# Performance work log

Measured on AMD Instinct MI355X. Metric: run time of the kernel, lower is better.

Reference implementation:

```python
import jax, jax.numpy as jnp
import numpy as np

QUERY_DIM = 512
KEY_DIM = 512
NUM_HEADS = 16
HEAD_DIM = QUERY_DIM // NUM_HEADS


def setup_inputs() -> dict:
    key = jax.random.key(0)
    ks = jax.random.split(key, 10)
    B, T, S = 4, 2048, 2048
    s_q = 1.0 / np.sqrt(QUERY_DIM)
    s_k = 1.0 / np.sqrt(KEY_DIM)
    return {
        "x": jax.random.normal(ks[0], (B, T, QUERY_DIM), dtype=jnp.float32),
        "context": jax.random.normal(ks[1], (B, S, KEY_DIM), dtype=jnp.float32),
        "Wq": jax.random.normal(ks[2], (QUERY_DIM, QUERY_DIM), dtype=jnp.float32) * s_q,
        "bq": jnp.zeros((QUERY_DIM,), dtype=jnp.float32),
        "Wk": jax.random.normal(ks[3], (KEY_DIM, QUERY_DIM), dtype=jnp.float32) * s_k,
        "bk": jnp.zeros((QUERY_DIM,), dtype=jnp.float32),
        "Wv": jax.random.normal(ks[4], (KEY_DIM, QUERY_DIM), dtype=jnp.float32) * s_k,
        "bv": jnp.zeros((QUERY_DIM,), dtype=jnp.float32),
        "Wo": jax.random.normal(ks[5], (QUERY_DIM, QUERY_DIM), dtype=jnp.float32) * s_q,
        "bo": jnp.zeros((QUERY_DIM,), dtype=jnp.float32),
    }


def reference(x, context, Wq, bq, Wk, bk, Wv, bv, Wo, bo):
    B, T, C = x.shape
    S = context.shape[1]
    H, D = NUM_HEADS, HEAD_DIM
    scale = D ** -0.5
    # projections -> [B, H, T/S, D]
    q = (x @ Wq + bq).reshape(B, T, H, D).transpose(0, 2, 1, 3)
    k = (context @ Wk + bk).reshape(B, S, H, D).transpose(0, 2, 1, 3)
    v = (context @ Wv + bv).reshape(B, S, H, D).transpose(0, 2, 1, 3)
    # explicit attention matrix [B, H, T, S] (faithful to the unfused original)
    attn = jnp.einsum("bhtd,bhsd->bhts", q, k) * scale
    attn = jax.nn.softmax(attn, axis=-1)  # dropout is identity in eval mode
    out = jnp.einsum("bhts,bhsd->bhtd", attn, v)
    out = out.transpose(0, 2, 1, 3).reshape(B, T, C)
    return out @ Wo + bo
```

## Files before the change

kernel.cpp:

```cpp
#include <hip/hip_runtime.h>
#include <hip/hip_bf16.h>
#include <cmath>

typedef __bf16 bf16;
typedef __bf16 bf16x2 __attribute__((ext_vector_type(2)));
typedef __bf16 bf16x4 __attribute__((ext_vector_type(4)));
typedef __bf16 bf16x8 __attribute__((ext_vector_type(8)));
typedef float floatx4 __attribute__((ext_vector_type(4)));

#define MFMA_BF16(a, b, c) __builtin_amdgcn_mfma_f32_16x16x32_bf16((a), (b), (c), 0, 0, 0)

#if defined(__has_builtin)
#if __has_builtin(__builtin_amdgcn_global_load_lds)
#define HAVE_GLL 1
#endif
#if __has_builtin(__builtin_amdgcn_cvt_pk_bf16_f32)
#define HAVE_PKCVT 1
#endif
#endif

__device__ __forceinline__ void stage16(const bf16* g, bf16* ldsbase, int lane) {
#ifdef HAVE_GLL
    __builtin_amdgcn_global_load_lds((const __attribute__((address_space(1))) unsigned int*)g,
                                     (__attribute__((address_space(3))) unsigned int*)ldsbase,
                                     16, 0, 0);
#else
    *(int4*)(ldsbase + lane * 8) = *(const int4*)g;
#endif
}

__device__ __forceinline__ bf16x4 pack4(float e0, float e1, float e2, float e3) {
#ifdef HAVE_PKCVT
    const bf16x2 lo = __builtin_amdgcn_cvt_pk_bf16_f32(e0, e1);
    const bf16x2 hi = __builtin_amdgcn_cvt_pk_bf16_f32(e2, e3);
    bf16x4 o;
    o[0] = lo[0]; o[1] = lo[1]; o[2] = hi[0]; o[3] = hi[1];
    return o;
#else
    bf16x4 o;
    o[0] = (bf16)e0; o[1] = (bf16)e1; o[2] = (bf16)e2; o[3] = (bf16)e3;
    return o;
#endif
}

__device__ __forceinline__ int detect_bf16(const void* x) {
    const unsigned short* u = (const unsigned short*)x;
    const int lane = threadIdx.x & 63;
    const unsigned short w0 = u[4 * lane], w1 = u[4 * lane + 2];
    const int e0 = (w0 >> 7) & 0xFF, e1 = (w1 >> 7) & 0xFF;
    const unsigned long long b0 = __ballot(e0 >= 96 && e0 <= 158);
    const unsigned long long b1 = __ballot(e1 >= 96 && e1 <= 158);
    return (__popcll(b0) + __popcll(b1)) >= 90;
}

struct PrepArgs {
    const void* x;
    const void* ctx;
    const void* W[4];
    const void* bias[4];
    bf16* xc;
    bf16* ctxc;
    bf16* WT[4];
    bf16* biasc;
};

__global__ __launch_bounds__(256) void prep(PrepArgs a) {
    const int tid = threadIdx.x;
    const int f = detect_bf16(a.x);
    const int bid = blockIdx.x;
    if (bid < 1024) {
        const int w = bid >> 8, tileid = bid & 255;
        const int bx = tileid & 15, by = tileid >> 4;
        const void* __restrict__ in = a.W[w];
        bf16* __restrict__ out = a.WT[w];
        __shared__ bf16 tile[32][33];
        const int tx = tid & 31, ty = tid >> 5;
        const int x = bx * 32 + tx;
        const int y0 = by * 32;
#pragma unroll
        for (int yy = ty; yy < 32; yy += 8) {
            const size_t idx = (size_t)(y0 + yy) * 512 + x;
            const float v = f ? (float)((const bf16*)in)[idx] : ((const float*)in)[idx];
            tile[yy][tx] = (bf16)v;
        }
        __syncthreads();
        const int xo = by * 32 + tx;
        const int y1 = bx * 32;
#pragma unroll
        for (int yy = ty; yy < 32; yy += 8)
            out[(size_t)(y1 + yy) * 512 + xo] = tile[tx][yy];
    } else if (bid < 5120) {
        if (f) return;
        const int seg = (bid >= 3072);
        const void* src = seg ? a.ctx : a.x;
        bf16* dst = seg ? a.ctxc : a.xc;
        const int off = (bid - (seg ? 3072 : 1024)) * 256 + tid;
        const float4 p = ((const float4*)src)[2 * off];
        const float4 q = ((const float4*)src)[2 * off + 1];
        bf16x8 o;
        o[0] = (bf16)p.x; o[1] = (bf16)p.y; o[2] = (bf16)p.z; o[3] = (bf16)p.w;
        o[4] = (bf16)q.x; o[5] = (bf16)q.y; o[6] = (bf16)q.z; o[7] = (bf16)q.w;
        *(bf16x8*)(dst + (size_t)off * 8) = o;
    } else {
        for (int e = tid; e < 2048; e += 256) {
            const int seg = e >> 9, off = e & 511;
            const float v =
                f ? (float)((const bf16*)a.bias[seg])[off] : ((const float*)a.bias[seg])[off];
            a.biasc[seg * 512 + off] = (bf16)v;
        }
    }
}

struct QkvArgs {
    const void* xraw;
    const void* ctxraw;
    const bf16* Aconv[3];
    const bf16* Wt[3];
    const bf16* bias;
    bf16* out[3];
    float scale[3];
};

__global__ __launch_bounds__(256) void gemm_qkv(QkvArgs a) {
    __shared__ __align__(16) bf16 lA[128 * 32];
    __shared__ __align__(16) bf16 lB[128 * 32];
    const int z = blockIdx.z;
    const int f = detect_bf16(a.xraw);
    const bf16* __restrict__ A =
        f ? (const bf16*)(z == 0 ? a.xraw : a.ctxraw) : a.Aconv[z];
    const bf16* __restrict__ Wt = a.Wt[z];
    const int tid = threadIdx.x, wave = tid >> 6, lane = tid & 63;
    const int qd = lane >> 4, j = lane & 15;
    const int m0 = blockIdx.x * 128, n0 = blockIdx.y * 128;
    const int wrow = (wave & 1) * 64, wcol = (wave >> 1) * 64;
    const int srow = wave * 16 + (lane >> 2);
    const int scol = (lane & 3) * 8;
    const bf16* agp = A + (size_t)(m0 + srow) * 512 + scol;
    const bf16* bgp = Wt + (size_t)(n0 + srow) * 512 + scol;
    bf16* lA0 = lA + wave * 512;
    bf16* lB0 = lB + wave * 512;

    floatx4 acc[4][4] = {};

    for (int k0 = 0; k0 < 512; k0 += 32) {
        stage16(agp + k0, lA0, lane);
        stage16(agp + k0 + (size_t)64 * 512, lA0 + 64 * 32, lane);
        stage16(bgp + k0, lB0, lane);
        stage16(bgp + k0 + (size_t)64 * 512, lB0 + 64 * 32, lane);
        __syncthreads();
        bf16x8 af[4], bfr[4];
#pragma unroll
        for (int i = 0; i < 4; ++i) {
            af[i] = *(const bf16x8*)(lA + (wrow + i * 16 + j) * 32 + qd * 8);
            bfr[i] = *(const bf16x8*)(lB + (wcol + i * 16 + j) * 32 + qd * 8);
        }
        if (z < 2) {
#pragma unroll
            for (int nt = 0; nt < 4; ++nt)
#pragma unroll
                for (int rf = 0; rf < 4; ++rf)
                    acc[nt][rf] = MFMA_BF16(bfr[nt], af[rf], acc[nt][rf]);
        } else {
#pragma unroll
            for (int rf = 0; rf < 4; ++rf)
#pragma unroll
                for (int nt = 0; nt < 4; ++nt)
                    acc[rf][nt] = MFMA_BF16(af[rf], bfr[nt], acc[rf][nt]);
        }
        __syncthreads();
    }

    const float scale = a.scale[z];
    const bf16* bias = a.bias + z * 512;
    bf16* __restrict__ C = a.out[z];
    if (z < 2) {
#pragma unroll
        for (int nt = 0; nt < 4; ++nt) {
            const int nb = n0 + wcol + nt * 16 + qd * 4;
            const bf16x4 bv4 = *(const bf16x4*)(bias + nb);
            const int h = nb >> 5, d0 = nb & 31;
#pragma unroll
            for (int rf = 0; rf < 4; ++rf) {
                const int m = m0 + wrow + rf * 16 + j;
                const int bb = m >> 11, t = m & 2047;
                bf16x4 pk;
#pragma unroll
                for (int r = 0; r < 4; ++r)
                    pk[r] = (bf16)((acc[nt][rf][r] + (float)bv4[r]) * scale);
                *(bf16x4*)(&C[(((size_t)bb * 16 + h) * 2048 + t) * 32 + d0]) = pk;
            }
        }
    } else {
#pragma unroll
        for (int nt = 0; nt < 4; ++nt) {
            const int n = n0 + wcol + nt * 16 + j;
            const float bv = (float)bias[n];
            const int h = n >> 5, d = n & 31;
#pragma unroll
            for (int rf = 0; rf < 4; ++rf) {
                const int t0 = m0 + wrow + rf * 16 + qd * 4;
                const int bb = t0 >> 11, s = t0 & 2047;
                bf16x4 pk;
#pragma unroll
                for (int r = 0; r < 4; ++r) pk[r] = (bf16)(acc[rf][nt][r] + bv);
                *(bf16x4*)(&C[(((size_t)bb * 16 + h) * 32 + d) * 2048 + s]) = pk;
            }
        }
    }
}

__global__ __launch_bounds__(256) void attn_kernel(const bf16* __restrict__ Q,
                                                   const bf16* __restrict__ Kh,
                                                   const bf16* __restrict__ Vt,
                                                   bf16* __restrict__ O) {
    const int tid = threadIdx.x;
    const int wave = tid >> 6, lane = tid & 63;
    const int qd = lane >> 4, j = lane & 15;
    const int bh = blockIdx.x;
    const int b = bh >> 4, h = bh & 15;
    const int tw = blockIdx.y * 256 + wave * 64;

    __shared__ __align__(16) bf16 lP[4][2 * 64 * 68];
    bf16* lp0 = lP[wave];
    bf16* lp1 = lP[wave] + 64 * 68;

    const bf16* qbase = Q + ((size_t)bh * 2048 + tw) * 32;
    const bf16* kbase = Kh + (size_t)bh * 2048 * 32;
    const bf16* vbase = Vt + (size_t)bh * 32 * 2048;

    bf16x8 qf[4];
#pragma unroll
    for (int tf = 0; tf < 4; ++tf)
        qf[tf] = *(const bf16x8*)(qbase + (size_t)(tf * 16 + j) * 32 + qd * 8);

    bf16x8 ones;
#pragma unroll
    for (int e = 0; e < 8; ++e) ones[e] = (bf16)1.0f;

    const floatx4 zero = {0.f, 0.f, 0.f, 0.f};
    floatx4 oacc[4][2] = {};
    floatx4 dacc[4] = {};

    bf16x8 K0[4], K1[4], V0[4], V1[4];

    auto loadK = [&](int s0, bf16x8* k) {
#pragma unroll
        for (int sf = 0; sf < 4; ++sf)
            k[sf] = *(const bf16x8*)(kbase + (size_t)(s0 + sf * 16 + j) * 32 + qd * 8);
    };
    auto loadV = [&](int s0, bf16x8* v) {
#pragma unroll
        for (int dt = 0; dt < 2; ++dt)
#pragma unroll
            for (int kk = 0; kk < 2; ++kk)
                v[dt * 2 + kk] =
                    *(const bf16x8*)(vbase + (size_t)(dt * 16 + j) * 2048 + s0 + kk * 32 + qd * 8);
    };
    auto qk = [&](bf16x8* k, bf16* lp) {
#pragma unroll
        for (int sf = 0; sf < 4; ++sf)
#pragma unroll
            for (int tf = 0; tf < 4; ++tf) {
                const floatx4 sc = MFMA_BF16(k[sf], qf[tf], zero);
                const float e0 = __builtin_amdgcn_exp2f(sc[0]);
                const float e1 = __builtin_amdgcn_exp2f(sc[1]);
                const float e2 = __builtin_amdgcn_exp2f(sc[2]);
                const float e3 = __builtin_amdgcn_exp2f(sc[3]);
                *(bf16x4*)(lp + (tf * 16 + j) * 68 + sf * 16 + qd * 4) = pack4(e0, e1, e2, e3);
            }
    };
    auto pv = [&](bf16x8* v, const bf16* lp) {
#pragma unroll
        for (int rf = 0; rf < 4; ++rf)
#pragma unroll
            for (int kk = 0; kk < 2; ++kk) {
                const bf16x8 pf = *(const bf16x8*)(lp + (rf * 16 + j) * 68 + kk * 32 + qd * 8);
#pragma unroll
                for (int dt = 0; dt < 2; ++dt)
                    oacc[rf][dt] = MFMA_BF16(pf, v[dt * 2 + kk], oacc[rf][dt]);
                dacc[rf] = MFMA_BF16(pf, ones, dacc[rf]);
            }
    };

    loadK(0, K0);
    loadV(0, V0);
    qk(K0, lp0);
    loadK(64, K1);
    for (int it = 0; it < 15; ++it) {
        loadV((2 * it + 1) * 64, V1);
        pv(V0, lp0);
        qk(K1, lp1);
        loadK((2 * it + 2) * 64, K0);
        loadV((2 * it + 2) * 64, V0);
        pv(V1, lp1);
        qk(K0, lp0);
        loadK((2 * it + 3) * 64, K1);
    }
    loadV(31 * 64, V1);
    pv(V0, lp0);
    qk(K1, lp1);
    pv(V1, lp1);

#pragma unroll
    for (int rf = 0; rf < 4; ++rf)
#pragma unroll
        for (int r = 0; r < 4; ++r) {
            const float inv = 1.0f / dacc[rf][r];
            const int t = tw + rf * 16 + qd * 4 + r;
#pragma unroll
            for (int dt = 0; dt < 2; ++dt)
                O[((size_t)b * 2048 + t) * 512 + h * 32 + dt * 16 + j] =
                    (bf16)(oacc[rf][dt][r] * inv);
        }
}

__global__ __launch_bounds__(256) void gemm_out(const bf16* __restrict__ A,
                                                const bf16* __restrict__ Wt,
                                                const bf16* __restrict__ bias,
                                                void* __restrict__ C,
                                                const void* __restrict__ xraw) {
    __shared__ __align__(16) bf16 lA[128 * 32];
    __shared__ __align__(16) bf16 lB[128 * 32];
    const int oflag = detect_bf16(xraw);
    const int tid = threadIdx.x, wave = tid >> 6, lane = tid & 63;
    const int qd = lane >> 4, j = lane & 15;
    const int m0 = blockIdx.x * 128, n0 = blockIdx.y * 128;
    const int wrow = (wave & 1) * 64, wcol = (wave >> 1) * 64;
    const int srow = wave * 16 + (lane >> 2);
    const int scol = (lane & 3) * 8;
    const bf16* agp = A + (size_t)(m0 + srow) * 512 + scol;
    const bf16* bgp = Wt + (size_t)(n0 + srow) * 512 + scol;
    bf16* lA0 = lA + wave * 512;
    bf16* lB0 = lB + wave * 512;

    floatx4 acc[4][4] = {};

    for (int k0 = 0; k0 < 512; k0 += 32) {
        stage16(agp + k0, lA0, lane);
        stage16(agp + k0 + (size_t)64 * 512, lA0 + 64 * 32, lane);
        stage16(bgp + k0, lB0, lane);
        stage16(bgp + k0 + (size_t)64 * 512, lB0 + 64 * 32, lane);
        __syncthreads();
        bf16x8 af[4], bfr[4];
#pragma unroll
        for (int i = 0; i < 4; ++i) {
            af[i] = *(const bf16x8*)(lA + (wrow + i * 16 + j) * 32 + qd * 8);
            bfr[i] = *(const bf16x8*)(lB + (wcol + i * 16 + j) * 32 + qd * 8);
        }
#pragma unroll
        for (int nt = 0; nt < 4; ++nt)
#pragma unroll
            for (int rf = 0; rf < 4; ++rf)
                acc[nt][rf] = MFMA_BF16(bfr[nt], af[rf], acc[nt][rf]);
        __syncthreads();
    }

#pragma unroll
    for (int nt = 0; nt < 4; ++nt) {
        const int nb = n0 + wcol + nt * 16 + qd * 4;
        const bf16x4 bv4 = *(const bf16x4*)(bias + nb);
#pragma unroll
        for (int rf = 0; rf < 4; ++rf) {
            const int m = m0 + wrow + rf * 16 + j;
            if (oflag) {
                bf16x4 pk;
#pragma unroll
                for (int r = 0; r < 4; ++r) pk[r] = (bf16)(acc[nt][rf][r] + (float)bv4[r]);
                *(bf16x4*)((bf16*)C + (size_t)m * 512 + nb) = pk;
            } else {
                float4 v;
                v.x = acc[nt][rf][0] + (float)bv4[0];
                v.y = acc[nt][rf][1] + (float)bv4[1];
                v.z = acc[nt][rf][2] + (float)bv4[2];
                v.w = acc[nt][rf][3] + (float)bv4[3];
                *(float4*)((float*)C + (size_t)m * 512 + nb) = v;
            }
        }
    }
}

extern "C" void kernel_launch(void* const* d_in, const int* in_sizes, int n_in, void* d_out,
                              int out_size, void* d_ws, size_t ws_size, hipStream_t stream) {
    char* ws = (char*)d_ws;
    bf16* wqT = (bf16*)(ws + 1048576);
    bf16* wkT = (bf16*)(ws + 1572864);
    bf16* wvT = (bf16*)(ws + 2097152);
    bf16* woT = (bf16*)(ws + 2621440);
    bf16* biasc = (bf16*)(ws + 3145728);
    bf16* xc = (bf16*)(ws + 4194304);
    bf16* ctxc = (bf16*)(ws + 12582912);
    bf16* qws = (bf16*)(ws + 20971520);
    bf16* kws = (bf16*)(ws + 29360128);
    bf16* vtws = (bf16*)(ws + 37748736);
    bf16* aws = xc;

    PrepArgs pa;
    pa.x = d_in[0]; pa.ctx = d_in[1];
    pa.W[0] = d_in[2]; pa.W[1] = d_in[4]; pa.W[2] = d_in[6]; pa.W[3] = d_in[8];
    pa.bias[0] = d_in[3]; pa.bias[1] = d_in[5]; pa.bias[2] = d_in[7]; pa.bias[3] = d_in[9];
    pa.xc = xc; pa.ctxc = ctxc;
    pa.WT[0] = wqT; pa.WT[1] = wkT; pa.WT[2] = wvT; pa.WT[3] = woT;
    pa.biasc = biasc;
    prep<<<5121, 256, 0, stream>>>(pa);

    QkvArgs qa;
    qa.xraw = d_in[0]; qa.ctxraw = d_in[1];
    qa.Aconv[0] = xc; qa.Aconv[1] = ctxc; qa.Aconv[2] = ctxc;
    qa.Wt[0] = wqT; qa.Wt[1] = wkT; qa.Wt[2] = wvT;
    qa.bias = biasc;
    qa.out[0] = qws; qa.out[1] = kws; qa.out[2] = vtws;
    qa.scale[0] = 0.2550348593f; qa.scale[1] = 1.0f; qa.scale[2] = 1.0f;
    gemm_qkv<<<dim3(64, 4, 3), 256, 0, stream>>>(qa);

    attn_kernel<<<dim3(64, 8), 256, 0, stream>>>(qws, kws, vtws, aws);

    gemm_out<<<dim3(64, 4), 256, 0, stream>>>(aws, woT, biasc + 3 * 512, d_out, d_in[0]);
}
```

Measured before the change: 216.3 us.

## Keep softmax probabilities in registers via permlane swaps instead of LDS round-trip

The attention kernel no longer writes exp'd scores to shared memory and reads them back as MFMA A-operands. It repacks them in registers with permlane32/permlane16 swaps. Each wave now covers 32 query rows instead of 64, the grid doubles in y, and launch bounds request 4 blocks per CU for occupancy. The manual double-buffered K/V prefetch pipeline is dropped for a simple loop, which relies on occupancy to hide load latency and halves K/V reuse per wave.

```diff
diff --git a/kernel.cpp b/kernel.cpp
--- a/kernel.cpp
+++ b/kernel.cpp
@@ -7,6 +7,8 @@
 typedef __bf16 bf16x4 __attribute__((ext_vector_type(4)));
 typedef __bf16 bf16x8 __attribute__((ext_vector_type(8)));
 typedef float floatx4 __attribute__((ext_vector_type(4)));
+typedef unsigned int uintx2 __attribute__((ext_vector_type(2)));
+typedef unsigned int uintx4 __attribute__((ext_vector_type(4)));
 
 #define MFMA_BF16(a, b, c) __builtin_amdgcn_mfma_f32_16x16x32_bf16((a), (b), (c), 0, 0, 0)
 
@@ -16,6 +18,9 @@
 #endif
 #if __has_builtin(__builtin_amdgcn_cvt_pk_bf16_f32)
 #define HAVE_PKCVT 1
+#endif
+#if __has_builtin(__builtin_amdgcn_permlane32_swap) && __has_builtin(__builtin_amdgcn_permlane16_swap)
+#define HAVE_PLSWAP 1
 #endif
 #endif
 
@@ -29,16 +34,49 @@
 #endif
 }
 
-__device__ __forceinline__ bf16x4 pack4(float e0, float e1, float e2, float e3) {
+__device__ __forceinline__ unsigned pk2(float a, float b) {
+    bf16x2 t;
 #ifdef HAVE_PKCVT
-    const bf16x2 lo = __builtin_amdgcn_cvt_pk_bf16_f32(e0, e1);
-    const bf16x2 hi = __builtin_amdgcn_cvt_pk_bf16_f32(e2, e3);
-    bf16x4 o;
-    o[0] = lo[0]; o[1] = lo[1]; o[2] = hi[0]; o[3] = hi[1];
+    t = __builtin_amdgcn_cvt_pk_bf16_f32(a, b);
+#else
+    t[0] = (bf16)a;
+    t[1] = (bf16)b;
+#endif
+    return __builtin_bit_cast(unsigned, t);
+}
+
+__device__ __forceinline__ uintx2 p32swap(unsigned x, unsigned y) {
+#ifdef HAVE_PLSWAP
+    auto r = __builtin_amdgcn_permlane32_swap(x, y, false, false);
+    uintx2 o;
+    o[0] = r[0];
+    o[1] = r[1];
     return o;
 #else
-    bf16x4 o;
-    o[0] = (bf16)e0; o[1] = (bf16)e1; o[2] = (bf16)e2; o[3] = (bf16)e3;
+    const int lane = threadIdx.x & 63;
+    const unsigned px = __shfl(x, lane ^ 32);
+    const unsigned py = __shfl(y, lane ^ 32);
+    uintx2 o;
+    o[0] = (lane & 32) ? py : x;
+    o[1] = (lane & 32) ? y : px;
+    return o;
+#endif
+}
+
+__device__ __forceinline__ uintx2 p16swap(unsigned x, unsigned y) {
+#ifdef HAVE_PLSWAP
+    auto r = __builtin_amdgcn_permlane16_swap(x, y, false, false);
+    uintx2 o;
+    o[0] = r[0];
+    o[1] = r[1];
+    return o;
+#else
+    const int lane = threadIdx.x & 63;
+    const unsigned px = __shfl(x, lane ^ 16);
+    const unsigned py = __shfl(y, lane ^ 16);
+    uintx2 o;
+    o[0] = (lane & 16) ? py : x;
+    o[1] = (lane & 16) ? y : px;
     return o;
 #endif
 }
@@ -209,28 +247,24 @@
     }
 }
 
-__global__ __launch_bounds__(256) void attn_kernel(const bf16* __restrict__ Q,
-                                                   const bf16* __restrict__ Kh,
-                                                   const bf16* __restrict__ Vt,
-                                                   bf16* __restrict__ O) {
+__global__ __launch_bounds__(256, 4) void attn_kernel(const bf16* __restrict__ Q,
+                                                      const bf16* __restrict__ Kh,
+                                                      const bf16* __restrict__ Vt,
+                                                      bf16* __restrict__ O) {
     const int tid = threadIdx.x;
     const int wave = tid >> 6, lane = tid & 63;
     const int qd = lane >> 4, j = lane & 15;
     const int bh = blockIdx.x;
     const int b = bh >> 4, h = bh & 15;
-    const int tw = blockIdx.y * 256 + wave * 64;
-
-    __shared__ __align__(16) bf16 lP[4][2 * 64 * 68];
-    bf16* lp0 = lP[wave];
-    bf16* lp1 = lP[wave] + 64 * 68;
+    const int tw = blockIdx.y * 128 + wave * 32;
 
     const bf16* qbase = Q + ((size_t)bh * 2048 + tw) * 32;
     const bf16* kbase = Kh + (size_t)bh * 2048 * 32;
     const bf16* vbase = Vt + (size_t)bh * 32 * 2048;
 
-    bf16x8 qf[4];
-#pragma unroll
-    for (int tf = 0; tf < 4; ++tf)
+    bf16x8 qf[2];
+#pragma unroll
+    for (int tf = 0; tf < 2; ++tf)
         qf[tf] = *(const bf16x8*)(qbase + (size_t)(tf * 16 + j) * 32 + qd * 8);
 
     bf16x8 ones;
@@ -238,79 +272,68 @@
     for (int e = 0; e < 8; ++e) ones[e] = (bf16)1.0f;
 
     const floatx4 zero = {0.f, 0.f, 0.f, 0.f};
-    floatx4 oacc[4][2] = {};
-    floatx4 dacc[4] = {};
-
-    bf16x8 K0[4], K1[4], V0[4], V1[4];
-
-    auto loadK = [&](int s0, bf16x8* k) {
+    floatx4 oacc[2][2] = {};
+    floatx4 dacc[2] = {};
+
+    for (int s0 = 0; s0 < 2048; s0 += 64) {
+        bf16x8 kf[4], vf[4];
 #pragma unroll
         for (int sf = 0; sf < 4; ++sf)
-            k[sf] = *(const bf16x8*)(kbase + (size_t)(s0 + sf * 16 + j) * 32 + qd * 8);
-    };
-    auto loadV = [&](int s0, bf16x8* v) {
+            kf[sf] = *(const bf16x8*)(kbase + (size_t)(s0 + sf * 16 + j) * 32 + qd * 8);
 #pragma unroll
         for (int dt = 0; dt < 2; ++dt)
 #pragma unroll
             for (int kk = 0; kk < 2; ++kk)
-                v[dt * 2 + kk] =
+                vf[dt * 2 + kk] =
                     *(const bf16x8*)(vbase + (size_t)(dt * 16 + j) * 2048 + s0 + kk * 32 + qd * 8);
-    };
-    auto qk = [&](bf16x8* k, bf16* lp) {
-#pragma unroll
-        for (int sf = 0; sf < 4; ++sf)
-#pragma unroll
-            for (int tf = 0; tf < 4; ++tf) {
-                const floatx4 sc = MFMA_BF16(k[sf], qf[tf], zero);
-                const float e0 = __builtin_amdgcn_exp2f(sc[0]);
-                const float e1 = __builtin_amdgcn_exp2f(sc[1]);
-                const float e2 = __builtin_amdgcn_exp2f(sc[2]);
-                const float e3 = __builtin_amdgcn_exp2f(sc[3]);
-                *(bf16x4*)(lp + (tf * 16 + j) * 68 + sf * 16 + qd * 4) = pack4(e0, e1, e2, e3);
+
+#pragma unroll
+        for (int tf = 0; tf < 2; ++tf) {
+            floatx4 sc[4];
+#pragma unroll
+            for (int sf = 0; sf < 4; ++sf) sc[sf] = MFMA_BF16(kf[sf], qf[tf], zero);
+            unsigned SW[4][2];
+#pragma unroll
+            for (int sf = 0; sf < 4; ++sf) {
+                const float e0 = __builtin_amdgcn_exp2f(sc[sf][0]);
+                const float e1 = __builtin_amdgcn_exp2f(sc[sf][1]);
+                const float e2 = __builtin_amdgcn_exp2f(sc[sf][2]);
+                const float e3 = __builtin_amdgcn_exp2f(sc[sf][3]);
+                SW[sf][0] = pk2(e0, e1);
+                SW[sf][1] = pk2(e2, e3);
             }
-    };
-    auto pv = [&](bf16x8* v, const bf16* lp) {
-#pragma unroll
-        for (int rf = 0; rf < 4; ++rf)
-#pragma unroll
-            for (int kk = 0; kk < 2; ++kk) {
-                const bf16x8 pf = *(const bf16x8*)(lp + (rf * 16 + j) * 68 + kk * 32 + qd * 8);
-#pragma unroll
-                for (int dt = 0; dt < 2; ++dt)
-                    oacc[rf][dt] = MFMA_BF16(pf, v[dt * 2 + kk], oacc[rf][dt]);
-                dacc[rf] = MFMA_BF16(pf, ones, dacc[rf]);
-            }
-    };
-
-    loadK(0, K0);
-    loadV(0, V0);
-    qk(K0, lp0);
-    loadK(64, K1);
-    for (int it = 0; it < 15; ++it) {
-        loadV((2 * it + 1) * 64, V1);
-        pv(V0, lp0);
-        qk(K1, lp1);
-        loadK((2 * it + 2) * 64, K0);
-        loadV((2 * it + 2) * 64, V0);
-        pv(V1, lp1);
-        qk(K0, lp0);
-        loadK((2 * it + 3) * 64, K1);
-    }
-    loadV(31 * 64, V1);
-    pv(V0, lp0);
-    qk(K1, lp1);
-    pv(V1, lp1);
-
-#pragma unroll
-    for (int rf = 0; rf < 4; ++rf)
+            const uintx2 a0 = p32swap(SW[0][0], SW[1][0]);
+            const uintx2 a1 = p32swap(SW[0][1], SW[1][1]);
+            const uintx2 c0 = p32swap(SW[2][0], SW[3][0]);
+            const uintx2 c1 = p32swap(SW[2][1], SW[3][1]);
+            const uintx2 t0 = p16swap(a0[0], a0[1]);
+            const uintx2 t1 = p16swap(a1[0], a1[1]);
+            const uintx2 t2 = p16swap(c0[0], c0[1]);
+            const uintx2 t3 = p16swap(c1[0], c1[1]);
+            uintx4 w0, w1;
+            w0[0] = t0[0]; w0[1] = t1[0]; w0[2] = t0[1]; w0[3] = t1[1];
+            w1[0] = t2[0]; w1[1] = t3[0]; w1[2] = t2[1]; w1[3] = t3[1];
+            const bf16x8 pf0 = __builtin_bit_cast(bf16x8, w0);
+            const bf16x8 pf1 = __builtin_bit_cast(bf16x8, w1);
+            oacc[tf][0] = MFMA_BF16(pf0, vf[0], oacc[tf][0]);
+            oacc[tf][1] = MFMA_BF16(pf0, vf[2], oacc[tf][1]);
+            dacc[tf] = MFMA_BF16(pf0, ones, dacc[tf]);
+            oacc[tf][0] = MFMA_BF16(pf1, vf[1], oacc[tf][0]);
+            oacc[tf][1] = MFMA_BF16(pf1, vf[3], oacc[tf][1]);
+            dacc[tf] = MFMA_BF16(pf1, ones, dacc[tf]);
+        }
+    }
+
+#pragma unroll
+    for (int tf = 0; tf < 2; ++tf)
 #pragma unroll
         for (int r = 0; r < 4; ++r) {
-            const float inv = 1.0f / dacc[rf][r];
-            const int t = tw + rf * 16 + qd * 4 + r;
+            const float inv = 1.0f / dacc[tf][r];
+            const int t = tw + tf * 16 + qd * 4 + r;
 #pragma unroll
             for (int dt = 0; dt < 2; ++dt)
                 O[((size_t)b * 2048 + t) * 512 + h * 32 + dt * 16 + j] =
-                    (bf16)(oacc[rf][dt][r] * inv);
+                    (bf16)(oacc[tf][dt][r] * inv);
         }
 }
 
@@ -412,7 +435,7 @@
     qa.scale[0] = 0.2550348593f; qa.scale[1] = 1.0f; qa.scale[2] = 1.0f;
     gemm_qkv<<<dim3(64, 4, 3), 256, 0, stream>>>(qa);
 
-    attn_kernel<<<dim3(64, 8), 256, 0, stream>>>(qws, kws, vtws, aws);
+    attn_kernel<<<dim3(64, 16), 256, 0, stream>>>(qws, kws, vtws, aws);
 
     gemm_out<<<dim3(64, 4), 256, 0, stream>>>(aws, woT, biasc + 3 * 512, d_out, d_in[0]);
 }
```

Result: slower. 230.1 us (+6.4%).
